# Optimization experiments

Hardware: AMD Instinct MI355X
Metric: run time of the kernel (lower is better)

The kernel has to match this reference:

```python
import jax, jax.numpy as jnp
import numpy as np

LN_EPS = 1e-5


def _layer_norm(x, g, b):
    m = jnp.mean(x, axis=-1, keepdims=True)
    v = jnp.mean(jnp.square(x - m), axis=-1, keepdims=True)
    return (x - m) * jax.lax.rsqrt(v + LN_EPS) * g + b


def _transition(x, g, bln, w_sw, w_ss, w_sig, b_sig, w_scale, residual):
    # TransitionBlock, eval mode (dropout = identity)
    x_in = x
    x = _layer_norm(x, g, bln)
    b = jax.nn.silu(x @ w_sw.T) * (x @ w_ss.T)
    y = jax.nn.sigmoid(x @ w_sig.T + b_sig) * (b @ w_scale.T)
    return x_in + y if residual else y


def setup_inputs() -> dict:
    N, E = 1000000, 100000
    F_DIM, A_DIM, H_DIM, HEADS = 64, 128, 256, 4
    D_IN = F_DIM + A_DIM
    key = jax.random.key(0)
    ks = jax.random.split(key, 16)
    s = 0.02
    inp = {
        'v_equivariant': jax.random.normal(ks[0], (N, 3), jnp.float32),
        'v_atom_features': jax.random.normal(ks[1], (N, A_DIM), jnp.float32),
        'edge_group_idx': jnp.sort(jax.random.randint(ks[2], (N,), 0, E)).astype(jnp.int32),
        'num_edges': E,
        'fourier_w': jax.random.normal(ks[3], (F_DIM,), jnp.float32),
        'fourier_b': jax.random.normal(ks[4], (F_DIM,), jnp.float32),
        # TransitionBlock 1 (input 192 -> 256, no residual)
        'tb1_ln_g': jnp.ones((D_IN,), jnp.float32),
        'tb1_ln_b': jnp.zeros((D_IN,), jnp.float32),
        'tb1_w_sw': jax.random.normal(ks[5], (H_DIM, D_IN), jnp.float32) * s,
        'tb1_w_ss': jax.random.normal(ks[6], (H_DIM, D_IN), jnp.float32) * s,
        'tb1_w_sig': jax.random.normal(ks[7], (H_DIM, D_IN), jnp.float32) * s,
        'tb1_b_sig': jnp.full((H_DIM,), -2.0, jnp.float32),
        'tb1_w_scale': jax.random.normal(ks[8], (H_DIM, H_DIM), jnp.float32) * s,
        # TransitionBlock 2 (256 -> 256, residual)
        'tb2_ln_g': jnp.ones((H_DIM,), jnp.float32),
        'tb2_ln_b': jnp.zeros((H_DIM,), jnp.float32),
        'tb2_w_sw': jax.random.normal(ks[9], (H_DIM, H_DIM), jnp.float32) * s,
        'tb2_w_ss': jax.random.normal(ks[10], (H_DIM, H_DIM), jnp.float32) * s,
        'tb2_w_sig': jax.random.normal(ks[11], (H_DIM, H_DIM), jnp.float32) * s,
        'tb2_b_sig': jnp.full((H_DIM,), -2.0, jnp.float32),
        'tb2_w_scale': jax.random.normal(ks[12], (H_DIM, H_DIM), jnp.float32) * s,
        # final linear 256 -> num_heads
        'out_w': jax.random.normal(ks[13], (HEADS, H_DIM), jnp.float32) * s,
        'out_b': jnp.zeros((HEADS,), jnp.float32),
    }
    return inp


def reference(v_equivariant, v_atom_features, edge_group_idx, num_edges,
              fourier_w, fourier_b,
              tb1_ln_g, tb1_ln_b, tb1_w_sw, tb1_w_ss, tb1_w_sig, tb1_b_sig, tb1_w_scale,
              tb2_ln_g, tb2_ln_b, tb2_w_sw, tb2_w_ss, tb2_w_sig, tb2_b_sig, tb2_w_scale,
              out_w, out_b):
    # Fourier embedding of vector norms: [N] -> [N, F_DIM]
    v_norms = jnp.linalg.norm(v_equivariant, axis=-1)
    f_dist = jnp.cos(2.0 * jnp.pi * (v_norms[..., None] * fourier_w + fourier_b))
    x = jnp.concatenate([f_dist, v_atom_features], axis=-1)  # [N, 192]
    x = _transition(x, tb1_ln_g, tb1_ln_b, tb1_w_sw, tb1_w_ss, tb1_w_sig, tb1_b_sig, tb1_w_scale, residual=False)
    x = _transition(x, tb2_ln_g, tb2_ln_b, tb2_w_sw, tb2_w_ss, tb2_w_sig, tb2_b_sig, tb2_w_scale, residual=True)
    scores = x @ out_w.T + out_b  # [N, H]
    # scatter_softmax over edge groups (per head)
    smax = jax.ops.segment_max(scores, edge_group_idx, num_segments=num_edges)
    e = jnp.exp(scores - smax[edge_group_idx])
    ssum = jax.ops.segment_sum(e, edge_group_idx, num_segments=num_edges)
    alphas = e / ssum[edge_group_idx]  # [N, H]
    # weighted scatter-sum pooling of 3-vectors per head
    v_weighted = v_equivariant[:, None, :] * alphas[..., None]  # [N, H, 3]
    v_pooled = jax.ops.segment_sum(v_weighted, edge_group_idx, num_segments=num_edges)
    return v_pooled.reshape(num_edges, -1)  # [E, H*3]
```

## Files before the change

### kernel.cpp

```cpp
#include <hip/hip_runtime.h>
#include <math.h>

#define DIN   192
#define HD    256
#define ROWS  64
#define THREADS 512
#define LSTR  256

typedef __bf16 bf16_t;
typedef bf16_t bf16x8 __attribute__((ext_vector_type(8)));
typedef float  f32x16 __attribute__((ext_vector_type(16)));

static __device__ __forceinline__ f32x16 mfma32(bf16x8 a, bf16x8 b, f32x16 c) {
  return __builtin_amdgcn_mfma_f32_32x32x16_bf16(a, b, c, 0, 0, 0);
}
static __device__ __forceinline__ unsigned short f2bfu(float f) {
  bf16_t h = (bf16_t)f; unsigned short u; __builtin_memcpy(&u, &h, 2); return u;
}
static __device__ __forceinline__ float bfu2f(unsigned short u) {
  unsigned x = ((unsigned)u) << 16; float f; __builtin_memcpy(&f, &x, 4); return f;
}
static __device__ __forceinline__ unsigned pk2(float a, float b) {
  return (unsigned)f2bfu(a) | ((unsigned)f2bfu(b) << 16);
}
static __device__ __forceinline__ float lo16(unsigned u) { return bfu2f((unsigned short)(u & 0xffff)); }
static __device__ __forceinline__ float hi16(unsigned u) { return bfu2f((unsigned short)(u >> 16)); }
static __device__ __forceinline__ float sigm(float x) {
  return __builtin_amdgcn_rcpf(1.f + __expf(-x));
}
static __device__ __forceinline__ int lidx(int row, int col) {
  return row * LSTR + (col ^ ((row & 7) << 3));
}
static __device__ __forceinline__ int crow(int r, int kg) {
  return (r & 3) + 8 * (r >> 2) + 4 * kg;
}

#define OFF_WSW1 0
#define OFF_WSS1 49152
#define OFF_WSG1 98304
#define OFF_WSC1 147456
#define OFF_WSW2 212992
#define OFF_WSS2 278528
#define OFF_WSG2 344064
#define OFF_WSC2 409600
#define OFF_WOUT 475136
#define NGRP_REORD 59392
#define NGRP_ALL   59520

__global__ void iab_wconv_kernel(const float* __restrict__ a0, const float* __restrict__ a1,
                                 const float* __restrict__ a2, const float* __restrict__ a3,
                                 const float* __restrict__ a4, const float* __restrict__ a5,
                                 const float* __restrict__ a6, const float* __restrict__ a7,
                                 const float* __restrict__ a8, unsigned short* __restrict__ out)
{
  const int i = blockIdx.x * 256 + threadIdx.x;
  if (i >= NGRP_ALL) return;
  if (i >= NGRP_REORD) {
    const int g = i - NGRP_REORD;
    #pragma unroll
    for (int j = 0; j < 8; ++j) out[OFF_WOUT + g * 8 + j] = f2bfu(a8[g * 8 + j]);
    return;
  }
  const float* src; int off, Kd, g;
  if      (i < 6144)  { src = a0; off = OFF_WSW1; Kd = 192; g = i; }
  else if (i < 12288) { src = a1; off = OFF_WSS1; Kd = 192; g = i - 6144; }
  else if (i < 18432) { src = a2; off = OFF_WSG1; Kd = 192; g = i - 12288; }
  else if (i < 26624) { src = a3; off = OFF_WSC1; Kd = 256; g = i - 18432; }
  else if (i < 34816) { src = a4; off = OFF_WSW2; Kd = 256; g = i - 26624; }
  else if (i < 43008) { src = a5; off = OFF_WSS2; Kd = 256; g = i - 34816; }
  else if (i < 51200) { src = a6; off = OFF_WSG2; Kd = 256; g = i - 43008; }
  else                { src = a7; off = OFF_WSC2; Kd = 256; g = i - 51200; }
  const int KS   = Kd >> 4;
  const int tile = g / (KS * 64);
  const int rem  = g - tile * (KS * 64);
  const int ks   = rem >> 6;
  const int ln   = rem & 63;
  const float* sp = src + (size_t)(tile * 32 + (ln & 31)) * Kd + ks * 16 + (ln >> 5) * 8;
  #pragma unroll
  for (int j = 0; j < 8; ++j) out[off + (size_t)g * 8 + j] = f2bfu(sp[j]);
}

template<int KS>
static __device__ __forceinline__ void gemm2(const unsigned short* __restrict__ Wt,
                                             const unsigned short* __restrict__ sIn,
                                             int l31, int kg, int xr,
                                             f32x16& acc0, f32x16& acc1)
{
  #pragma unroll 4
  for (int ks = 0; ks < KS; ++ks) {
    const bf16x8 Wc = *(const bf16x8*)(Wt + ks * 512);
    const int col = (ks * 16 + kg * 8) ^ xr;
    const bf16x8 A0 = *(const bf16x8*)(sIn + l31 * LSTR + col);
    const bf16x8 A1 = *(const bf16x8*)(sIn + (l31 + 32) * LSTR + col);
    acc0 = mfma32(A0, Wc, acc0);
    acc1 = mfma32(A1, Wc, acc1);
  }
}

static __device__ __forceinline__ void pack32(const f32x16 a0, const f32x16 a1, unsigned* up)
{
  #pragma unroll
  for (int p = 0; p < 8; ++p) up[p]     = pk2(a0[2 * p], a0[2 * p + 1]);
  #pragma unroll
  for (int p = 0; p < 8; ++p) up[8 + p] = pk2(a1[2 * p], a1[2 * p + 1]);
}

static __device__ __forceinline__ void storeSilu(unsigned short* dst, const unsigned* up,
                                                 const f32x16 s, int mt, int kg, int ocol)
{
  #pragma unroll
  for (int p = 0; p < 8; ++p) {
    const float ua = lo16(up[p]), ub = hi16(up[p]);
    const int r0 = 2 * p;
    const int row0 = mt * 32 + crow(r0, kg);
    dst[lidx(row0,     ocol)] = f2bfu(ua * sigm(ua) * s[r0]);
    dst[lidx(row0 + 1, ocol)] = f2bfu(ub * sigm(ub) * s[r0 + 1]);
  }
}

static __device__ __forceinline__ void storePk(unsigned short* dst, const unsigned* xp,
                                               int kg, int ocol)
{
  #pragma unroll
  for (int mt = 0; mt < 2; ++mt) {
    #pragma unroll
    for (int p = 0; p < 8; ++p) {
      const int r0 = 2 * p;
      const int row0 = mt * 32 + crow(r0, kg);
      const unsigned pk = xp[mt * 8 + p];
      dst[lidx(row0,     ocol)] = (unsigned short)(pk & 0xffff);
      dst[lidx(row0 + 1, ocol)] = (unsigned short)(pk >> 16);
    }
  }
}

__global__ __launch_bounds__(THREADS, 2)
void iab_rows_mfma(
    const float* __restrict__ v, const float* __restrict__ af,
    const float* __restrict__ fw, const float* __restrict__ fb,
    const float* __restrict__ ln1g, const float* __restrict__ ln1b,
    const float* __restrict__ bsig1,
    const float* __restrict__ ln2g, const float* __restrict__ ln2b,
    const float* __restrict__ bsig2,
    const float* __restrict__ outb,
    const unsigned short* __restrict__ wc,
    float* __restrict__ scores, int N)
{
  __shared__ __align__(16) unsigned short sA[ROWS * LSTR];
  __shared__ __align__(16) unsigned short sB[ROWS * LSTR];

  const int t    = threadIdx.x;
  const int w    = t >> 6;
  const int lane = t & 63;
  const int l31  = lane & 31;
  const int kg   = lane >> 5;
  const int xr   = (lane & 7) << 3;
  const int ocol = w * 32 + l31;
  const int row0 = blockIdx.x * ROWS;

  const unsigned short* WtSW1 = wc + OFF_WSW1 + (w * 12 * 64 + lane) * 8;
  const unsigned short* WtSS1 = wc + OFF_WSS1 + (w * 12 * 64 + lane) * 8;
  const unsigned short* WtSG1 = wc + OFF_WSG1 + (w * 12 * 64 + lane) * 8;
  const unsigned short* WtSC1 = wc + OFF_WSC1 + (w * 16 * 64 + lane) * 8;
  const unsigned short* WtSW2 = wc + OFF_WSW2 + (w * 16 * 64 + lane) * 8;
  const unsigned short* WtSS2 = wc + OFF_WSS2 + (w * 16 * 64 + lane) * 8;
  const unsigned short* WtSG2 = wc + OFF_WSG2 + (w * 16 * 64 + lane) * 8;
  const unsigned short* WtSC2 = wc + OFF_WSC2 + (w * 16 * 64 + lane) * 8;

  {
    const float fwl = fw[lane], fbl = fb[lane];
    const float g1a = ln1g[lane], g1b = ln1g[lane + 64], g1c = ln1g[lane + 128];
    const float o1a = ln1b[lane], o1b = ln1b[lane + 64], o1c = ln1b[lane + 128];
    for (int rr = 0; rr < 8; ++rr) {
      const int r = w * 8 + rr;
      const int g = row0 + r;
      float e0 = 0.f, e1 = 0.f, e2 = 0.f;
      if (g < N) {
        const float vx = v[3 * (size_t)g + 0];
        const float vy = v[3 * (size_t)g + 1];
        const float vz = v[3 * (size_t)g + 2];
        const float nrm = sqrtf(vx * vx + vy * vy + vz * vz);
        e0 = __cosf(6.283185307179586f * (nrm * fwl + fbl));
        const float* a = af + (size_t)g * 128;
        e1 = a[lane];
        e2 = a[lane + 64];
      }
      float s  = e0 + e1 + e2;
      float sq = e0 * e0 + e1 * e1 + e2 * e2;
      #pragma unroll
      for (int o = 32; o >= 1; o >>= 1) {
        s  += __shfl_xor(s,  o);
        sq += __shfl_xor(sq, o);
      }
      const float mean = s * (1.f / 192.f);
      const float var  = fmaxf(sq * (1.f / 192.f) - mean * mean, 0.f);
      const float rstd = rsqrtf(var + 1e-5f);
      sA[lidx(r, lane)]       = f2bfu((e0 - mean) * rstd * g1a + o1a);
      sA[lidx(r, lane + 64)]  = f2bfu((e1 - mean) * rstd * g1b + o1b);
      sA[lidx(r, lane + 128)] = f2bfu((e2 - mean) * rstd * g1c + o1c);
    }
  }
  __syncthreads();

  unsigned x2p[16];

  {
    unsigned up[16];
    {
      f32x16 u0{}, u1{};
      gemm2<12>(WtSW1, sA, l31, kg, xr, u0, u1);
      pack32(u0, u1, up);
    }
    f32x16 s0{}, s1{};
    gemm2<12>(WtSS1, sA, l31, kg, xr, s0, s1);
    storeSilu(sB, up,     s0, 0, kg, ocol);
    storeSilu(sB, up + 8, s1, 1, kg, ocol);
  }

  unsigned sgp[16];
  {
    f32x16 g0{}, g1{};
    gemm2<12>(WtSG1, sA, l31, kg, xr, g0, g1);
    const float bias = bsig1[ocol];
    #pragma unroll
    for (int p = 0; p < 8; ++p) {
      sgp[p]     = pk2(sigm(g0[2*p] + bias), sigm(g0[2*p+1] + bias));
      sgp[8 + p] = pk2(sigm(g1[2*p] + bias), sigm(g1[2*p+1] + bias));
    }
  }
  __syncthreads();

  {
    f32x16 c0{}, c1{};
    gemm2<16>(WtSC1, sB, l31, kg, xr, c0, c1);
    #pragma unroll
    for (int p = 0; p < 8; ++p) {
      x2p[p]     = pk2(lo16(sgp[p]) * c0[2*p],     hi16(sgp[p]) * c0[2*p+1]);
      x2p[8 + p] = pk2(lo16(sgp[8+p]) * c1[2*p],   hi16(sgp[8+p]) * c1[2*p+1]);
    }
    storePk(sA, x2p, kg, ocol);
  }
  __syncthreads();

  {
    float g2v[4], o2v[4];
    #pragma unroll
    for (int i = 0; i < 4; ++i) { g2v[i] = ln2g[lane + 64 * i]; o2v[i] = ln2b[lane + 64 * i]; }
    for (int rr = 0; rr < 8; ++rr) {
      const int r = w * 8 + rr;
      float e[4];
      #pragma unroll
      for (int i = 0; i < 4; ++i) e[i] = bfu2f(sA[lidx(r, lane + 64 * i)]);
      float s  = e[0] + e[1] + e[2] + e[3];
      float sq = e[0]*e[0] + e[1]*e[1] + e[2]*e[2] + e[3]*e[3];
      #pragma unroll
      for (int o = 32; o >= 1; o >>= 1) {
        s  += __shfl_xor(s,  o);
        sq += __shfl_xor(sq, o);
      }
      const float mean = s * (1.f / 256.f);
      const float var  = fmaxf(sq * (1.f / 256.f) - mean * mean, 0.f);
      const float rstd = rsqrtf(var + 1e-5f);
      #pragma unroll
      for (int i = 0; i < 4; ++i)
        sA[lidx(r, lane + 64 * i)] = f2bfu((e[i] - mean) * rstd * g2v[i] + o2v[i]);
    }
  }
  __syncthreads();

  {
    unsigned up[16];
    {
      f32x16 u0{}, u1{};
      gemm2<16>(WtSW2, sA, l31, kg, xr, u0, u1);
      pack32(u0, u1, up);
    }
    f32x16 s0{}, s1{};
    gemm2<16>(WtSS2, sA, l31, kg, xr, s0, s1);
    storeSilu(sB, up,     s0, 0, kg, ocol);
    storeSilu(sB, up + 8, s1, 1, kg, ocol);
  }

  {
    f32x16 g0{}, g1{};
    gemm2<16>(WtSG2, sA, l31, kg, xr, g0, g1);
    const float bias = bsig2[ocol];
    #pragma unroll
    for (int p = 0; p < 8; ++p) {
      sgp[p]     = pk2(sigm(g0[2*p] + bias), sigm(g0[2*p+1] + bias));
      sgp[8 + p] = pk2(sigm(g1[2*p] + bias), sigm(g1[2*p+1] + bias));
    }
  }
  __syncthreads();

  {
    f32x16 c0{}, c1{};
    gemm2<16>(WtSC2, sB, l31, kg, xr, c0, c1);
    #pragma unroll
    for (int p = 0; p < 8; ++p) {
      x2p[p]     = pk2(lo16(x2p[p])   + lo16(sgp[p])   * c0[2*p],
                       hi16(x2p[p])   + hi16(sgp[p])   * c0[2*p+1]);
      x2p[8 + p] = pk2(lo16(x2p[8+p]) + lo16(sgp[8+p]) * c1[2*p],
                       hi16(x2p[8+p]) + hi16(sgp[8+p]) * c1[2*p+1]);
    }
    storePk(sA, x2p, kg, ocol);
  }
  __syncthreads();

  if (t < ROWS * 4) {
    const int r = t >> 2;
    const int h = t & 3;
    const int g = row0 + r;
    if (g < N) {
      float acc = outb[h];
      const int xrr = (r & 7) << 3;
      const unsigned short* rp = sA + r * LSTR;
      const unsigned short* wp = wc + OFF_WOUT + h * HD;
      #pragma unroll
      for (int s = 0; s < 32; ++s) {
        bf16x8 x  = *(const bf16x8*)(rp + ((s * 8) ^ xrr));
        bf16x8 ww = *(const bf16x8*)(wp + s * 8);
        #pragma unroll
        for (int j = 0; j < 8; ++j) acc += (float)x[j] * (float)ww[j];
      }
      scores[(size_t)g * 4 + h] = acc;
    }
  }
}

__device__ __forceinline__ int iab_lower_bound(const int* __restrict__ a, int n, int key)
{
  int lo = 0, hi = n;
  while (lo < hi) {
    const int mid = (lo + hi) >> 1;
    if (a[mid] < key) lo = mid + 1; else hi = mid;
  }
  return lo;
}

__global__ __launch_bounds__(256)
void iab_segpool_kernel(const float* __restrict__ scores,
                        const float* __restrict__ v,
                        const int* __restrict__ gidx,
                        float* __restrict__ out, int N, int E)
{
  const int seg  = blockIdx.x * 4 + (threadIdx.x >> 6);
  const int lane = threadIdx.x & 63;
  if (seg >= E) return;

  const int lo = iab_lower_bound(gidx, N, seg);
  const int hi = iab_lower_bound(gidx, N, seg + 1);

  const int h  = lane & 3;
  const int ro = lane >> 2;

  float m = -INFINITY;
  for (int base = lo; base < hi; base += 16) {
    const int r = base + ro;
    if (r < hi) m = fmaxf(m, scores[(size_t)r * 4 + h]);
  }
  #pragma unroll
  for (int o = 4; o < 64; o <<= 1) m = fmaxf(m, __shfl_xor(m, o));

  float ssum = 0.f, w0 = 0.f, w1 = 0.f, w2 = 0.f;
  for (int base = lo; base < hi; base += 16) {
    const int r = base + ro;
    if (r < hi) {
      const float e = expf(scores[(size_t)r * 4 + h] - m);
      ssum += e;
      w0 += e * v[3 * (size_t)r + 0];
      w1 += e * v[3 * (size_t)r + 1];
      w2 += e * v[3 * (size_t)r + 2];
    }
  }
  #pragma unroll
  for (int o = 4; o < 64; o <<= 1) {
    ssum += __shfl_xor(ssum, o);
    w0   += __shfl_xor(w0, o);
    w1   += __shfl_xor(w1, o);
    w2   += __shfl_xor(w2, o);
  }

  if (ro == 0) {
    const float inv = (hi > lo) ? (1.f / ssum) : 0.f;
    out[(size_t)seg * 12 + h * 3 + 0] = w0 * inv;
    out[(size_t)seg * 12 + h * 3 + 1] = w1 * inv;
    out[(size_t)seg * 12 + h * 3 + 2] = w2 * inv;
  }
}

extern "C" void kernel_launch(void* const* d_in, const int* in_sizes, int n_in,
                              void* d_out, int out_size, void* d_ws, size_t ws_size,
                              hipStream_t stream)
{
  const float* v     = (const float*)d_in[0];
  const float* af    = (const float*)d_in[1];
  const int*   gidx  = (const int*)  d_in[2];
  const float* fw    = (const float*)d_in[4];
  const float* fb    = (const float*)d_in[5];
  const float* ln1g  = (const float*)d_in[6];
  const float* ln1b  = (const float*)d_in[7];
  const float* wsw1  = (const float*)d_in[8];
  const float* wss1  = (const float*)d_in[9];
  const float* wsig1 = (const float*)d_in[10];
  const float* bsig1 = (const float*)d_in[11];
  const float* wsc1  = (const float*)d_in[12];
  const float* ln2g  = (const float*)d_in[13];
  const float* ln2b  = (const float*)d_in[14];
  const float* wsw2  = (const float*)d_in[15];
  const float* wss2  = (const float*)d_in[16];
  const float* wsig2 = (const float*)d_in[17];
  const float* bsig2 = (const float*)d_in[18];
  const float* wsc2  = (const float*)d_in[19];
  const float* outw  = (const float*)d_in[20];
  const float* outb  = (const float*)d_in[21];

  const int N = in_sizes[0] / 3;
  const int E = out_size / 12;

  float* scores = (float*)d_ws;
  unsigned short* wcv = (unsigned short*)((char*)d_ws + (size_t)N * 4 * sizeof(float));

  hipLaunchKernelGGL(iab_wconv_kernel, dim3((NGRP_ALL + 255) / 256), dim3(256), 0, stream,
                     wsw1, wss1, wsig1, wsc1, wsw2, wss2, wsig2, wsc2, outw, wcv);

  hipLaunchKernelGGL(iab_rows_mfma, dim3((N + ROWS - 1) / ROWS), dim3(THREADS), 0, stream,
                     v, af, fw, fb, ln1g, ln1b, bsig1, ln2g, ln2b, bsig2, outb,
                     wcv, scores, N);

  hipLaunchKernelGGL(iab_segpool_kernel, dim3((E + 3) / 4), dim3(256), 0, stream,
                     scores, v, gidx, (float*)d_out, N, E);
}
```

Baseline: 2.058 ms.

## Interleave SiLU and gate GEMMs and compute output head with MFMA

Fuses the two GEMMs sharing the same LDS input (swish and scale branches) into one loop that reads each input tile once and issues four MFMAs per step. This drops the intermediate bf16 packing of the swish result and keeps it in fp32. The final 256->4 projection now uses a zero-padded 32-column MFMA tile on two waves instead of scalar dot products on 256 threads, and the weight-conversion kernel is extended to write that padded layout. This adds accumulator register pressure, which could lower occupancy.

```diff
diff --git a/kernel.cpp b/kernel.cpp
--- a/kernel.cpp
+++ b/kernel.cpp
@@ -45,7 +45,7 @@
 #define OFF_WSC2 409600
 #define OFF_WOUT 475136
 #define NGRP_REORD 59392
-#define NGRP_ALL   59520
+#define NGRP_ALL   60416
 
 __global__ void iab_wconv_kernel(const float* __restrict__ a0, const float* __restrict__ a1,
                                  const float* __restrict__ a2, const float* __restrict__ a3,
@@ -56,9 +56,16 @@
   const int i = blockIdx.x * 256 + threadIdx.x;
   if (i >= NGRP_ALL) return;
   if (i >= NGRP_REORD) {
-    const int g = i - NGRP_REORD;
-    #pragma unroll
-    for (int j = 0; j < 8; ++j) out[OFF_WOUT + g * 8 + j] = f2bfu(a8[g * 8 + j]);
+    const int g  = i - NGRP_REORD;
+    const int ks = g >> 6;
+    const int ln = g & 63;
+    const int col = ln & 31;
+    const int kg  = ln >> 5;
+    #pragma unroll
+    for (int j = 0; j < 8; ++j) {
+      const float vv = (col < 4) ? a8[col * 256 + ks * 16 + kg * 8 + j] : 0.f;
+      out[OFF_WOUT + (size_t)g * 8 + j] = f2bfu(vv);
+    }
     return;
   }
   const float* src; int off, Kd, g;
@@ -97,24 +104,35 @@
   }
 }
 
-static __device__ __forceinline__ void pack32(const f32x16 a0, const f32x16 a1, unsigned* up)
+template<int KS>
+static __device__ __forceinline__ void gemm2p(const unsigned short* __restrict__ Wa,
+                                              const unsigned short* __restrict__ Wb,
+                                              const unsigned short* __restrict__ sIn,
+                                              int l31, int kg, int xr,
+                                              f32x16& u0, f32x16& u1,
+                                              f32x16& s0, f32x16& s1)
+{
+  #pragma unroll 2
+  for (int ks = 0; ks < KS; ++ks) {
+    const bf16x8 wa = *(const bf16x8*)(Wa + ks * 512);
+    const bf16x8 wb = *(const bf16x8*)(Wb + ks * 512);
+    const int col = (ks * 16 + kg * 8) ^ xr;
+    const bf16x8 A0 = *(const bf16x8*)(sIn + l31 * LSTR + col);
+    const bf16x8 A1 = *(const bf16x8*)(sIn + (l31 + 32) * LSTR + col);
+    u0 = mfma32(A0, wa, u0);
+    s0 = mfma32(A0, wb, s0);
+    u1 = mfma32(A1, wa, u1);
+    s1 = mfma32(A1, wb, s1);
+  }
+}
+
+static __device__ __forceinline__ void storeSilu2(unsigned short* dst, const f32x16 u,
+                                                  const f32x16 s, int mt, int kg, int ocol)
 {
   #pragma unroll
-  for (int p = 0; p < 8; ++p) up[p]     = pk2(a0[2 * p], a0[2 * p + 1]);
-  #pragma unroll
-  for (int p = 0; p < 8; ++p) up[8 + p] = pk2(a1[2 * p], a1[2 * p + 1]);
-}
-
-static __device__ __forceinline__ void storeSilu(unsigned short* dst, const unsigned* up,
-                                                 const f32x16 s, int mt, int kg, int ocol)
-{
-  #pragma unroll
-  for (int p = 0; p < 8; ++p) {
-    const float ua = lo16(up[p]), ub = hi16(up[p]);
-    const int r0 = 2 * p;
-    const int row0 = mt * 32 + crow(r0, kg);
-    dst[lidx(row0,     ocol)] = f2bfu(ua * sigm(ua) * s[r0]);
-    dst[lidx(row0 + 1, ocol)] = f2bfu(ub * sigm(ub) * s[r0 + 1]);
+  for (int i = 0; i < 16; ++i) {
+    const float x = u[i];
+    dst[lidx(mt * 32 + crow(i, kg), ocol)] = f2bfu(x * sigm(x) * s[i]);
   }
 }
 
@@ -205,16 +223,10 @@
   unsigned x2p[16];
 
   {
-    unsigned up[16];
-    {
-      f32x16 u0{}, u1{};
-      gemm2<12>(WtSW1, sA, l31, kg, xr, u0, u1);
-      pack32(u0, u1, up);
-    }
-    f32x16 s0{}, s1{};
-    gemm2<12>(WtSS1, sA, l31, kg, xr, s0, s1);
-    storeSilu(sB, up,     s0, 0, kg, ocol);
-    storeSilu(sB, up + 8, s1, 1, kg, ocol);
+    f32x16 u0{}, u1{}, s0{}, s1{};
+    gemm2p<12>(WtSW1, WtSS1, sA, l31, kg, xr, u0, u1, s0, s1);
+    storeSilu2(sB, u0, s0, 0, kg, ocol);
+    storeSilu2(sB, u1, s1, 1, kg, ocol);
   }
 
   unsigned sgp[16];
@@ -235,8 +247,8 @@
     gemm2<16>(WtSC1, sB, l31, kg, xr, c0, c1);
     #pragma unroll
     for (int p = 0; p < 8; ++p) {
-      x2p[p]     = pk2(lo16(sgp[p]) * c0[2*p],     hi16(sgp[p]) * c0[2*p+1]);
-      x2p[8 + p] = pk2(lo16(sgp[8+p]) * c1[2*p],   hi16(sgp[8+p]) * c1[2*p+1]);
+      x2p[p]     = pk2(lo16(sgp[p])   * c0[2*p], hi16(sgp[p])   * c0[2*p+1]);
+      x2p[8 + p] = pk2(lo16(sgp[8+p]) * c1[2*p], hi16(sgp[8+p]) * c1[2*p+1]);
     }
     storePk(sA, x2p, kg, ocol);
   }
@@ -269,16 +281,10 @@
   __syncthreads();
 
   {
-    unsigned up[16];
-    {
-      f32x16 u0{}, u1{};
-      gemm2<16>(WtSW2, sA, l31, kg, xr, u0, u1);
-      pack32(u0, u1, up);
-    }
-    f32x16 s0{}, s1{};
-    gemm2<16>(WtSS2, sA, l31, kg, xr, s0, s1);
-    storeSilu(sB, up,     s0, 0, kg, ocol);
-    storeSilu(sB, up + 8, s1, 1, kg, ocol);
+    f32x16 u0{}, u1{}, s0{}, s1{};
+    gemm2p<16>(WtSW2, WtSS2, sA, l31, kg, xr, u0, u1, s0, s1);
+    storeSilu2(sB, u0, s0, 0, kg, ocol);
+    storeSilu2(sB, u1, s1, 1, kg, ocol);
   }
 
   {
@@ -307,23 +313,23 @@
   }
   __syncthreads();
 
-  if (t < ROWS * 4) {
-    const int r = t >> 2;
-    const int h = t & 3;
-    const int g = row0 + r;
-    if (g < N) {
-      float acc = outb[h];
-      const int xrr = (r & 7) << 3;
-      const unsigned short* rp = sA + r * LSTR;
-      const unsigned short* wp = wc + OFF_WOUT + h * HD;
+  if (w < 2) {
+    const unsigned short* WtF = wc + OFF_WOUT + (size_t)lane * 8;
+    f32x16 c{};
+    #pragma unroll 4
+    for (int ks = 0; ks < 16; ++ks) {
+      const bf16x8 wf = *(const bf16x8*)(WtF + ks * 512);
+      const int col = (ks * 16 + kg * 8) ^ xr;
+      const bf16x8 A = *(const bf16x8*)(sA + (w * 32 + l31) * LSTR + col);
+      c = mfma32(A, wf, c);
+    }
+    if (l31 < 4) {
+      const float bias = outb[l31];
       #pragma unroll
-      for (int s = 0; s < 32; ++s) {
-        bf16x8 x  = *(const bf16x8*)(rp + ((s * 8) ^ xrr));
-        bf16x8 ww = *(const bf16x8*)(wp + s * 8);
-        #pragma unroll
-        for (int j = 0; j < 8; ++j) acc += (float)x[j] * (float)ww[j];
+      for (int i = 0; i < 16; ++i) {
+        const int g = row0 + w * 32 + crow(i, kg);
+        if (g < N) scores[(size_t)g * 4 + l31] = c[i] + bias;
       }
-      scores[(size_t)g * 4 + h] = acc;
     }
   }
 }
```

Result: faster. 1.948 ms (-5.3%).
